# Performance work log

Hardware: AMD Instinct MI355X
Metric: run time of the kernel (lower is better)

Reference implementation:

```python
import jax, jax.numpy as jnp
import numpy as np

N = 20000   # nodes
E = 320000  # edges per relation
R = 4       # relations
H = 4       # attention heads
HID = 64    # hidden_dim1
DIN = 256   # input_dim
OUT = 64    # output_dim
NEG_SLOPE = 0.2  # PyG GATv2Conv default


def setup_inputs() -> dict:
    key = jax.random.key(0)
    ks = jax.random.split(key, 16)
    rn = lambda k, s: jax.random.normal(k, s, jnp.float32) * 0.05
    return {
        "x": jax.random.normal(ks[0], (N, DIN), jnp.float32),
        "edge_indices": jax.random.randint(ks[1], (R, 2, E), 0, N, jnp.int32),
        "Wl1": rn(ks[2], (R, DIN, H * HID)),
        "Wr1": rn(ks[3], (R, DIN, H * HID)),
        "att1": rn(ks[4], (R, H, HID)),
        "b1": rn(ks[5], (R, H * HID)),
        "Wl2": rn(ks[6], (R, H * HID, H * HID)),
        "Wr2": rn(ks[7], (R, H * HID, H * HID)),
        "att2": rn(ks[8], (R, H, HID)),
        "b2": rn(ks[9], (R, H * HID)),
        "Wrel3": rn(ks[10], (R, H * HID, HID)),
        "Wroot3": rn(ks[11], (R, H * HID, HID)),
        "b3": rn(ks[12], (R, HID)),
        "Wrel4": rn(ks[13], (R, HID, OUT)),
        "Wroot4": rn(ks[14], (R, HID, OUT)),
        "b4": rn(ks[15], (R, OUT)),
    }


def gatv2(x, src, dst, Wl, Wr, att, bias):
    """PyG GATv2Conv (concat heads, add_self_loops=True, share_weights=False)."""
    n = x.shape[0]
    loop = jnp.arange(n, dtype=src.dtype)
    src = jnp.concatenate([src, loop])  # add self loops
    dst = jnp.concatenate([dst, loop])
    xl = (x @ Wl).reshape(n, H, -1)  # source transform [N,H,C]
    xr = (x @ Wr).reshape(n, H, -1)  # target transform [N,H,C]
    z = jax.nn.leaky_relu(xl[src] + xr[dst], NEG_SLOPE)  # [E',H,C]
    e = jnp.einsum('ehc,hc->eh', z, att)                 # per-edge logits
    m = jax.ops.segment_max(e, dst, num_segments=n)
    m = jnp.where(jnp.isfinite(m), m, 0.0)
    p = jnp.exp(e - m[dst])
    s = jax.ops.segment_sum(p, dst, num_segments=n)
    alpha = p / s[dst]                                   # segment softmax
    out = jax.ops.segment_sum(alpha[:, :, None] * xl[src], dst, num_segments=n)
    return out.reshape(n, -1) + bias


def graphconv(x, src, dst, Wrel, Wroot, b):
    """PyG GraphConv: W1 x_i + W2 sum_j x_j (aggr='add')."""
    agg = jax.ops.segment_sum(x[src], dst, num_segments=x.shape[0])
    return agg @ Wrel + b + x @ Wroot


def reference(x, edge_indices, Wl1, Wr1, att1, b1, Wl2, Wr2, att2, b2,
              Wrel3, Wroot3, b3, Wrel4, Wroot4, b4):
    outs = []
    for i in range(R):  # small fixed relation count
        src, dst = edge_indices[i, 0], edge_indices[i, 1]
        h = jax.nn.relu(gatv2(x, src, dst, Wl1[i], Wr1[i], att1[i], b1[i]))
        h = jax.nn.relu(gatv2(h, src, dst, Wl2[i], Wr2[i], att2[i], b2[i]))
        h = jax.nn.relu(graphconv(h, src, dst, Wrel3[i], Wroot3[i], b3[i]))
        h = graphconv(h, src, dst, Wrel4[i], Wroot4[i], b4[i])
        outs.append(h[:, None, :])
    return jnp.concatenate(outs, axis=1)  # [N, R, OUT]
```

## Files before the change

kernel.cpp:

```cpp
#include <hip/hip_runtime.h>
#include <hip/hip_fp16.h>
#include <math.h>

#define NN   20000
#define EE   320000
#define RR   4
#define NBKT 4
#define BKTW 5000
#define SM   (NBKT*NN)
#define SB   40
#define SE   2000

typedef unsigned short u16;
typedef unsigned int   u32;
typedef _Float16 half8v __attribute__((ext_vector_type(8)));
typedef _Float16 v2h    __attribute__((ext_vector_type(2)));
typedef __attribute__((ext_vector_type(4))) float f32x4;

static __device__ __forceinline__ u16 f2h(float f){ return __half_as_ushort(__float2half_rn(f)); }
static __device__ __forceinline__ v2h u2v(u32 u){ union{u32 u; v2h v;} c; c.u=u; return c.v; }
static __device__ __forceinline__ u32 v2u(v2h v){ union{u32 u; v2h v;} c; c.v=v; return c.u; }
static __device__ __forceinline__ v2h splat2(float f){ v2h r; r[0]=(_Float16)f; r[1]=(_Float16)f; return r; }
static __device__ __forceinline__ float fdot2(v2h a, v2h b, float c){
  return __builtin_amdgcn_fdot2(a, b, c, false);
}
static __device__ __forceinline__ void gload_lds16(const void* g, void* l){
  __builtin_amdgcn_global_load_lds((const __attribute__((address_space(1))) void*)g,
                                   (__attribute__((address_space(3))) void*)l, 16, 0, 0);
}

__global__ void k_countA(const int* __restrict__ ei, int* __restrict__ degb){
  int i = blockIdx.x*blockDim.x + threadIdx.x;
  if (i < RR*EE) {
    int r = i / EE, e = i % EE;
    int s = ei[(size_t)r*2*EE + e];
    int d = ei[(size_t)r*2*EE + EE + e];
    int b = s / BKTW;
    atomicAdd(&degb[((size_t)r*NN + d)*NBKT + b], 1);
  }
}
__global__ __launch_bounds__(256) void k_scanA(const int* __restrict__ degb, int* __restrict__ bsum){
  int r = blockIdx.x / SB, b = blockIdx.x % SB;
  const int* p = degb + (size_t)r*SM + b*SE;
  int t = threadIdx.x;
  int s = 0;
  for (int i = t; i < SE; i += 256) s += p[i];
  s += __shfl_xor(s,1); s += __shfl_xor(s,2); s += __shfl_xor(s,4);
  s += __shfl_xor(s,8); s += __shfl_xor(s,16); s += __shfl_xor(s,32);
  __shared__ int ws[4];
  if ((t & 63) == 0) ws[t >> 6] = s;
  __syncthreads();
  if (t == 0) bsum[blockIdx.x] = ws[0] + ws[1] + ws[2] + ws[3];
}
__global__ void k_scanB(int* __restrict__ bsum, int* __restrict__ off_all){
  int r = blockIdx.x;
  if (threadIdx.x == 0) {
    int run = 0;
    for (int b = 0; b < SB; ++b) {
      int v = bsum[r*SB + b];
      bsum[r*SB + b] = run;
      run += v;
    }
    off_all[(size_t)r*(SM+1) + SM] = run;
  }
}
__global__ __launch_bounds__(256) void k_scanC(const int* __restrict__ degb, const int* __restrict__ bsum,
                                               int* __restrict__ off_all, int* __restrict__ cur_all){
  int r = blockIdx.x / SB, b = blockIdx.x % SB;
  const int* p = degb + (size_t)r*SM + b*SE;
  int* off = off_all + (size_t)r*(SM+1) + b*SE;
  int* cur = cur_all + (size_t)r*SM + b*SE;
  int t = threadIdx.x;
  int base_i = t*8;
  int v[8]; int tot = 0;
  if (base_i < SE) {
    #pragma unroll
    for (int j = 0; j < 8; ++j) { v[j] = p[base_i + j]; tot += v[j]; }
  }
  __shared__ int part[256];
  part[t] = tot;
  __syncthreads();
  for (int d = 1; d < 256; d <<= 1) {
    int u = (t >= d) ? part[t-d] : 0;
    __syncthreads();
    part[t] += u;
    __syncthreads();
  }
  if (base_i < SE) {
    int run = bsum[r*SB + b] + ((t == 0) ? 0 : part[t-1]);
    #pragma unroll
    for (int j = 0; j < 8; ++j) {
      off[base_i + j] = run;
      cur[base_i + j] = run;
      run += v[j];
    }
  }
}
__global__ void k_scatterM(const int* __restrict__ ei, int* __restrict__ curb, u32* __restrict__ csr4){
  int bid = blockIdx.x;
  int pass = bid / 5000;
  int i = (bid - pass*5000)*256 + threadIdx.x;
  int dlo = pass*5000, dhi = dlo + 5000;
  if (i < RR*EE) {
    int r = i / EE, e = i - r*EE;
    int d = ei[(size_t)r*2*EE + EE + e];
    if (d >= dlo && d < dhi) {
      int s = ei[(size_t)r*2*EE + e];
      int b = s / BKTW;
      int p = atomicAdd(&curb[((size_t)r*NN + d)*NBKT + b], 1);
      csr4[(size_t)r*EE + p] = (u32)s * 4096u;
    }
  }
}

__global__ void k_prepx(const float* __restrict__ x, u16* __restrict__ xbf, int* __restrict__ degb){
  int kind = blockIdx.y;
  int i = blockIdx.x*256 + threadIdx.x;
  if (kind == 0) {
    if (i < NN*256/4) {
      float4 v = reinterpret_cast<const float4*>(x)[i];
      ushort4 b;
      b.x = f2h(v.x); b.y = f2h(v.y); b.z = f2h(v.z); b.w = f2h(v.w);
      reinterpret_cast<ushort4*>(xbf)[i] = b;
    }
  } else {
    if (i < RR*SM) degb[i] = 0;
  }
}

__global__ __launch_bounds__(256) void k_wtrans(
    const float* __restrict__ A1, const float* __restrict__ B1, u16* __restrict__ D1,
    const float* __restrict__ A2, const float* __restrict__ B2, u16* __restrict__ D2,
    const float* __restrict__ A3, const float* __restrict__ B3, u16* __restrict__ D3,
    const float* __restrict__ A4, const float* __restrict__ B4, u16* __restrict__ D4)
{
  int kind = blockIdx.z;
  int K, N; const float *A, *B; u16* D;
  if (kind == 0)      { K=256; N=256; A=A1; B=B1; D=D1; }
  else if (kind == 1) { K=256; N=256; A=A2; B=B2; D=D2; }
  else if (kind == 2) { K=256; N=64;  A=A3; B=B3; D=D3; }
  else                { K=64;  N=64;  A=A4; B=B4; D=D4; }
  const int tiles_n = N >> 6;
  const int tiles = (K >> 6) * tiles_n;
  const int tile = blockIdx.x;
  if (tile >= tiles) return;
  const int r = blockIdx.y >> 1, half = blockIdx.y & 1;
  const float* S = half ? B : A;
  const int tk = tile / tiles_n, tn = tile % tiles_n;
  __shared__ u16 ts[64][66];
  const int t = threadIdx.x;
  #pragma unroll
  for (int i = 0; i < 16; ++i) {
    int lin = i*256 + t;
    int row = lin >> 6, col = lin & 63;
    ts[row][col] = f2h(S[((size_t)r*K + tk*64 + row)*N + tn*64 + col]);
  }
  __syncthreads();
  #pragma unroll
  for (int i = 0; i < 16; ++i) {
    int lin = i*256 + t;
    int nrow = lin >> 6, kcol = lin & 63;
    D[((size_t)r*2*N + half*N + tn*64 + nrow)*K + tk*64 + kcol] = ts[kcol][nrow];
  }
}

__global__ __launch_bounds__(256) void k_mfma(
    const u16* __restrict__ A, const u16* __restrict__ BT,
    int M, int K, u16* __restrict__ Cb, int ldc,
    long aZ, long btZ, long cZ, int nby, int nz)
{
  constexpr int BM = 128, BN = 128;
  constexpr int FI = 4, FJ = 4;
  constexpr int CH = 20;
  const int bid = blockIdx.x;
  const int xcd = bid & 7;
  const int u   = bid >> 3;
  const int nbz = nby*nz;
  const int byz = u % nbz;
  const int bxi = u / nbz;
  const int bx  = xcd*CH + bxi;
  const int bm  = bx * BM;
  if (bm >= M) return;
  const int by  = byz % nby;
  const int zz  = byz / nby;
  const int bn  = by * BN;
  A  += (size_t)zz*aZ;
  BT += (size_t)zz*btZ;
  Cb += (size_t)zz*cZ;

  __shared__ u16 As[BM*32];
  __shared__ u16 Bs[BN*32];
  const int t = threadIdx.x;
  const int lane = t & 63, wid = t >> 6;
  const int wr = wid >> 1, wc = wid & 1;
  const int lr = lane & 15, lk = lane >> 4;

  f32x4 acc[FI][FJ];
  #pragma unroll
  for (int i = 0; i < FI; ++i)
    #pragma unroll
    for (int j = 0; j < FJ; ++j) acc[i][j] = (f32x4)(0.f);

  const int nk = K >> 5;
  char* AsB = (char*)As;
  char* BsB = (char*)Bs;

  for (int s = 0; s < nk; ++s) {
    const int kk = s << 5;
    #pragma unroll
    for (int i = 0; i < 2; ++i) {
      int c = t + 256*i;
      int row = c >> 2, sub = c & 3;
      int lsub = sub ^ (row & 3);
      int grow = bm + row; if (grow >= M) grow = M - 1;
      gload_lds16(A + (size_t)grow*K + kk + lsub*8, AsB + c*16);
    }
    #pragma unroll
    for (int i = 0; i < 2; ++i) {
      int c = t + 256*i;
      int row = c >> 2, sub = c & 3;
      int lsub = sub ^ (row & 3);
      gload_lds16(BT + (size_t)(bn + row)*K + kk + lsub*8, BsB + c*16);
    }
    __syncthreads();
    half8v a[FI], b[FJ];
    #pragma unroll
    for (int i = 0; i < FI; ++i) {
      int row = wr*64 + i*16 + lr;
      int sub = lk ^ (row & 3);
      a[i] = *reinterpret_cast<half8v*>(AsB + row*64 + sub*16);
    }
    #pragma unroll
    for (int j = 0; j < FJ; ++j) {
      int col = wc*64 + j*16 + lr;
      int sub = lk ^ (col & 3);
      b[j] = *reinterpret_cast<half8v*>(BsB + col*64 + sub*16);
    }
    #pragma unroll
    for (int i = 0; i < FI; ++i)
      #pragma unroll
      for (int j = 0; j < FJ; ++j)
        acc[i][j] = __builtin_amdgcn_mfma_f32_16x16x32_f16(a[i], b[j], acc[i][j], 0, 0, 0);
    __syncthreads();
  }

  #pragma unroll
  for (int i = 0; i < FI; ++i) {
    #pragma unroll
    for (int j = 0; j < FJ; ++j) {
      int col = bn + wc*64 + j*16 + lr;
      #pragma unroll
      for (int q = 0; q < 4; ++q) {
        int row = bm + wr*64 + i*16 + lk*4 + q;
        if (row < M) Cb[(size_t)row*ldc + col] = f2h(acc[i][j][q]);
      }
    }
  }
}

__global__ __launch_bounds__(256) void k_gat(
    const u16* __restrict__ xlr,
    const float* __restrict__ att, const float* __restrict__ bias,
    const int* __restrict__ offb4, const u32* __restrict__ csr4,
    u16* __restrict__ out)
{
  const int bid = blockIdx.x;
  const int z = (bid & 7) >> 1;
  const int j4 = ((bid >> 3) << 1) | (bid & 1);
  const int node = j4*4 + (threadIdx.x >> 6);
  if (node >= NN) return;
  const int lane = threadIdx.x & 63;
  const int sl = lane & 31, sub = lane >> 5;
  const int* offb = offb4 + (size_t)z*(SM+1);
  const u32* csr = csr4 + (size_t)z*EE;
  u16* outp = out + (size_t)z*(size_t)NN*256;

  const int co = sl*8;
  const char* xc = (const char*)xlr + (size_t)z*1024 + co*2;
  const u16* selfrow = xlr + (size_t)z*512 + (size_t)node*2048;
  const v2h c02 = splat2(0.2f);
  const float L2E = 1.4426950408889634f;

  uint4 rx = *reinterpret_cast<const uint4*>(selfrow + 256 + co);
  v2h xr2[4] = {u2v(rx.x), u2v(rx.y), u2v(rx.z), u2v(rx.w)};
  v2h av2[4];
  {
    float4 q0 = *reinterpret_cast<const float4*>(att + z*256 + co);
    float4 q1 = *reinterpret_cast<const float4*>(att + z*256 + co + 4);
    av2[0][0]=(_Float16)(q0.x*L2E); av2[0][1]=(_Float16)(q0.y*L2E);
    av2[1][0]=(_Float16)(q0.z*L2E); av2[1][1]=(_Float16)(q0.w*L2E);
    av2[2][0]=(_Float16)(q1.x*L2E); av2[2][1]=(_Float16)(q1.y*L2E);
    av2[3][0]=(_Float16)(q1.z*L2E); av2[3][1]=(_Float16)(q1.w*L2E);
  }
  uint4 sx = *reinterpret_cast<const uint4*>(selfrow + co);
  v2h xs2[4] = {u2v(sx.x), u2v(sx.y), u2v(sx.z), u2v(sx.w)};
  float ps = 0.f;
  #pragma unroll
  for (int i = 0; i < 4; ++i) {
    v2h zz = xs2[i] + xr2[i];
    v2h lr = __builtin_elementwise_max(zz, zz*c02);
    ps = fdot2(av2[i], lr, ps);
  }
  ps += __shfl_xor(ps,1); ps += __shfl_xor(ps,2); ps += __shfl_xor(ps,4);
  float wsf = (sub == 0) ? exp2f(fminf(ps - 6.f, 12.f)) : 0.f;
  float s = wsf;
  v2h a2[4];
  {
    v2h w2 = splat2(wsf);
    #pragma unroll
    for (int i = 0; i < 4; ++i) a2[i] = w2*xs2[i];
  }

  const int e0 = offb[node*NBKT], e1 = offb[node*NBKT + NBKT];
  const int kfull = e0 + ((e1 - e0) & ~7);
  for (int k = e0; k < kfull; k += 8) {
    v2h xv[4][4];
    float p[4];
    #pragma unroll
    for (int j = 0; j < 4; ++j) {
      u32 boff = csr[k + 2*j + sub];
      uint4 v = *reinterpret_cast<const uint4*>(xc + boff);
      xv[j][0]=u2v(v.x); xv[j][1]=u2v(v.y); xv[j][2]=u2v(v.z); xv[j][3]=u2v(v.w);
      float pp = 0.f;
      #pragma unroll
      for (int i = 0; i < 4; ++i) {
        v2h zz = xv[j][i] + xr2[i];
        v2h lr = __builtin_elementwise_max(zz, zz*c02);
        pp = fdot2(av2[i], lr, pp);
      }
      p[j] = pp;
    }
    #pragma unroll
    for (int j = 0; j < 4; ++j) {
      p[j] += __shfl_xor(p[j],1);
      p[j] += __shfl_xor(p[j],2);
      p[j] += __shfl_xor(p[j],4);
    }
    float w[4];
    #pragma unroll
    for (int j = 0; j < 4; ++j) w[j] = exp2f(fminf(p[j] - 6.f, 12.f));
    s += (w[0] + w[1]) + (w[2] + w[3]);
    #pragma unroll
    for (int j = 0; j < 4; ++j) {
      v2h w2 = splat2(w[j]);
      #pragma unroll
      for (int i = 0; i < 4; ++i) a2[i] += w2*xv[j][i];
    }
  }
  for (int k = kfull; k < e1; k += 2) {
    int kk = k + sub;
    bool val = kk < e1;
    u32 boff = csr[val ? kk : e1-1];
    uint4 v = *reinterpret_cast<const uint4*>(xc + boff);
    v2h xv[4] = {u2v(v.x), u2v(v.y), u2v(v.z), u2v(v.w)};
    float pp = 0.f;
    #pragma unroll
    for (int i = 0; i < 4; ++i) {
      v2h zz = xv[i] + xr2[i];
      v2h lr = __builtin_elementwise_max(zz, zz*c02);
      pp = fdot2(av2[i], lr, pp);
    }
    pp += __shfl_xor(pp,1); pp += __shfl_xor(pp,2); pp += __shfl_xor(pp,4);
    float w = val ? exp2f(fminf(pp - 6.f, 12.f)) : 0.f;
    s += w;
    v2h w2 = splat2(w);
    #pragma unroll
    for (int i = 0; i < 4; ++i) a2[i] += w2*xv[i];
  }
  s += __shfl_xor(s, 32);
  #pragma unroll
  for (int i = 0; i < 4; ++i) {
    u32 t = (u32)__shfl_xor((int)v2u(a2[i]), 32);
    a2[i] += u2v(t);
  }
  float inv = 1.f / s;
  if (sub == 0) {
    float4 b0 = *reinterpret_cast<const float4*>(bias + z*256 + co);
    float4 b1 = *reinterpret_cast<const float4*>(bias + z*256 + co + 4);
    float bv[8] = {b0.x,b0.y,b0.z,b0.w,b1.x,b1.y,b1.z,b1.w};
    u32 o[4];
    #pragma unroll
    for (int i = 0; i < 4; ++i) {
      float lo = fmaxf((float)a2[i][0]*inv + bv[2*i],   0.f);
      float hi = fmaxf((float)a2[i][1]*inv + bv[2*i+1], 0.f);
      o[i] = (u32)f2h(lo) | ((u32)f2h(hi) << 16);
    }
    uint4 ov = {o[0], o[1], o[2], o[3]};
    *reinterpret_cast<uint4*>(outp + (size_t)node*256 + co) = ov;
  }
}

template<int RELU, int F32OUT>
__global__ __launch_bounds__(256) void k_aggp(
    const u16* __restrict__ C, const float* __restrict__ bias,
    const int* __restrict__ offb4, const u32* __restrict__ csr4,
    u16* __restrict__ outb, float* __restrict__ outf)
{
  const int bid = blockIdx.x;
  const int z = (bid & 7) >> 1;
  const int j4 = ((bid >> 3) << 1) | (bid & 1);
  const int node = j4*4 + (threadIdx.x >> 6);
  if (node >= NN) return;
  const int lane = threadIdx.x & 63;
  const int g = lane >> 4, sl = lane & 15;
  const u16* Cp = C + (size_t)z*(size_t)NN*128;
  const char* Cc = (const char*)Cp + sl*8;
  const int* offb = offb4 + (size_t)z*(SM+1);
  const u32* csr = csr4 + (size_t)z*EE;
  const int co = sl*4;
  v2h acc0 = splat2(0.f), acc1 = splat2(0.f);
  const int e0 = offb[node*NBKT], e1 = offb[node*NBKT + NBKT];
  const int kfull = e0 + ((e1 - e0) & ~7);
  for (int k = e0; k < kfull; k += 8) {
    #pragma unroll
    for (int j = 0; j < 2; ++j) {
      u32 boff = csr[k + 2*g + j] >> 4;
      uint2 v = *reinterpret_cast<const uint2*>(Cc + boff);
      acc0 += u2v(v.x);
      acc1 += u2v(v.y);
    }
  }
  for (int k = kfull; k < e1; k += 4) {
    int kk = k + g;
    bool val = kk < e1;
    u32 boff = csr[val ? kk : e1-1] >> 4;
    uint2 v = *reinterpret_cast<const uint2*>(Cc + boff);
    acc0 += u2v(val ? v.x : 0u);
    acc1 += u2v(val ? v.y : 0u);
  }
  float a0 = (float)acc0[0], a1 = (float)acc0[1];
  float a2 = (float)acc1[0], a3 = (float)acc1[1];
  a0 += __shfl_xor(a0,16); a1 += __shfl_xor(a1,16);
  a2 += __shfl_xor(a2,16); a3 += __shfl_xor(a3,16);
  a0 += __shfl_xor(a0,32); a1 += __shfl_xor(a1,32);
  a2 += __shfl_xor(a2,32); a3 += __shfl_xor(a3,32);
  if (g == 0) {
    uint2 q = *reinterpret_cast<const uint2*>(Cp + (size_t)node*128 + 64 + co);
    v2h q0 = u2v(q.x), q1 = u2v(q.y);
    float4 bv = *reinterpret_cast<const float4*>(bias + z*64 + co);
    float v0 = a0 + (float)q0[0] + bv.x;
    float v1 = a1 + (float)q0[1] + bv.y;
    float v2 = a2 + (float)q1[0] + bv.z;
    float v3 = a3 + (float)q1[1] + bv.w;
    if (RELU) {
      v0 = fmaxf(v0, 0.f); v1 = fmaxf(v1, 0.f);
      v2 = fmaxf(v2, 0.f); v3 = fmaxf(v3, 0.f);
    }
    if (F32OUT) {
      float4 o = {v0, v1, v2, v3};
      *reinterpret_cast<float4*>(outf + (size_t)node*256 + z*64 + co) = o;
    } else {
      uint2 o;
      o.x = (u32)f2h(v0) | ((u32)f2h(v1) << 16);
      o.y = (u32)f2h(v2) | ((u32)f2h(v3) << 16);
      *reinterpret_cast<uint2*>(outb + ((size_t)z*NN + node)*64 + co) = o;
    }
  }
}

extern "C" void kernel_launch(void* const* d_in, const int* in_sizes, int n_in,
                              void* d_out, int out_size, void* d_ws, size_t ws_size,
                              hipStream_t stream)
{
  const float* x      = (const float*)d_in[0];
  const int*   ei     = (const int*)  d_in[1];
  const float* Wl1    = (const float*)d_in[2];
  const float* Wr1    = (const float*)d_in[3];
  const float* att1   = (const float*)d_in[4];
  const float* b1     = (const float*)d_in[5];
  const float* Wl2    = (const float*)d_in[6];
  const float* Wr2    = (const float*)d_in[7];
  const float* att2   = (const float*)d_in[8];
  const float* b2     = (const float*)d_in[9];
  const float* Wrel3  = (const float*)d_in[10];
  const float* Wroot3 = (const float*)d_in[11];
  const float* b3     = (const float*)d_in[12];
  const float* Wrel4  = (const float*)d_in[13];
  const float* Wroot4 = (const float*)d_in[14];
  const float* b4     = (const float*)d_in[15];
  float* out = (float*)d_out;

  const dim3 thr(256);
  const size_t NB2048 = (size_t)NN*2048;
  const size_t NB256  = (size_t)NN*256;
  const size_t NB128  = (size_t)NN*128;
  const size_t NB64   = (size_t)NN*64;

  u16* XLR = (u16*)d_ws;
  u16* h   = XLR + NB2048;
  u16* xbf = h   + NB256*RR;
  u16* W1T = xbf + NB256;
  u16* W2T = W1T + (size_t)RR*512*256;
  u16* W3T = W2T + (size_t)RR*512*256;
  u16* W4T = W3T + (size_t)RR*128*256;
  int* degb = (int*)(W4T + (size_t)RR*128*64);
  int* offb = degb + (size_t)RR*SM;
  int* curb = offb + (size_t)RR*(SM+1);
  u32* csr4 = (u32*)(curb + (size_t)RR*SM);
  int* bsum = (int*)(csr4 + (size_t)RR*EE);
  u16* C34 = XLR;
  u16* h3b = XLR + NB128*RR;

  k_prepx <<<dim3(5000,2), thr, 0, stream>>>(x, xbf, degb);
  k_wtrans<<<dim3(16,8,4), thr, 0, stream>>>(Wl1, Wr1, W1T, Wl2, Wr2, W2T,
                                             Wrel3, Wroot3, W3T, Wrel4, Wroot4, W4T);

  k_countA <<<dim3((RR*EE+255)/256), thr, 0, stream>>>(ei, degb);
  k_scanA  <<<dim3(RR*SB), thr, 0, stream>>>(degb, bsum);
  k_scanB  <<<dim3(RR), dim3(64), 0, stream>>>(bsum, offb);
  k_scanC  <<<dim3(RR*SB), thr, 0, stream>>>(degb, bsum, offb, curb);
  k_scatterM<<<dim3(20000), thr, 0, stream>>>(ei, curb, csr4);

  const dim3 gNode(20000);
  k_mfma<<<dim3(8*20*16), thr, 0, stream>>>(xbf, W1T, NN, 256, XLR, 2048, 0, 0, 0, 16, 1);
  k_gat<<<gNode, thr, 0, stream>>>(XLR, att1, b1, offb, csr4, h);
  k_mfma<<<dim3(8*20*16), thr, 0, stream>>>(h, W2T, NN, 256, XLR, 2048,
                                            (long)NB256, 512*256, 512, 4, 4);
  k_gat<<<gNode, thr, 0, stream>>>(XLR, att2, b2, offb, csr4, h);
  k_mfma<<<dim3(8*20*4), thr, 0, stream>>>(h, W3T, NN, 256, C34, 128,
                                           (long)NB256, 128*256, (long)NB128, 1, 4);
  k_aggp<1,0><<<gNode, thr, 0, stream>>>(C34, b3, offb, csr4, h3b, nullptr);
  k_mfma<<<dim3(8*20*4), thr, 0, stream>>>(h3b, W4T, NN, 64, C34, 128,
                                           (long)NB64, 128*64, (long)NB128, 1, 4);
  k_aggp<0,1><<<gNode, thr, 0, stream>>>(C34, b4, offb, csr4, nullptr, out);
}
```

Measured before the change: 484.8 us.

## Merge prep kernels, fold scanB into scanC, use nontemporal loads/stores

Merges the x-to-fp16 conversion, degree-buffer clearing and weight transposition into one launch, and folds the serial block-offset scan into scanC, where thread 0 of each block sums the preceding block totals. Together these remove two kernel launches and a tiny single-threaded kernel from the dependency chain. It also switches some per-node loads and stores in the GAT and aggregation kernels to nontemporal builtins so streaming data bypasses cache retention. The risk is that each scanC block now rereads the block sums redundantly, and the nontemporal hints could hurt if that data is reused soon after.

```diff
diff --git a/kernel.cpp b/kernel.cpp
--- a/kernel.cpp
+++ b/kernel.cpp
@@ -15,6 +15,8 @@
 typedef unsigned int   u32;
 typedef _Float16 half8v __attribute__((ext_vector_type(8)));
 typedef _Float16 v2h    __attribute__((ext_vector_type(2)));
+typedef u32 u32x4 __attribute__((ext_vector_type(4)));
+typedef u32 u32x2 __attribute__((ext_vector_type(2)));
 typedef __attribute__((ext_vector_type(4))) float f32x4;
 
 static __device__ __forceinline__ u16 f2h(float f){ return __half_as_ushort(__float2half_rn(f)); }
@@ -27,6 +29,61 @@
 static __device__ __forceinline__ void gload_lds16(const void* g, void* l){
   __builtin_amdgcn_global_load_lds((const __attribute__((address_space(1))) void*)g,
                                    (__attribute__((address_space(3))) void*)l, 16, 0, 0);
+}
+
+__global__ __launch_bounds__(256) void k_prep(
+    const float* __restrict__ x, u16* __restrict__ xbf, int* __restrict__ degb,
+    const float* __restrict__ A1, const float* __restrict__ B1, u16* __restrict__ D1,
+    const float* __restrict__ A2, const float* __restrict__ B2, u16* __restrict__ D2,
+    const float* __restrict__ A3, const float* __restrict__ B3, u16* __restrict__ D3,
+    const float* __restrict__ A4, const float* __restrict__ B4, u16* __restrict__ D4)
+{
+  __shared__ u16 ts[64][66];
+  const int bid = blockIdx.x;
+  const int t = threadIdx.x;
+  if (bid < 10000) {
+    int kind = bid / 5000;
+    int i = (bid % 5000)*256 + t;
+    if (kind == 0) {
+      if (i < NN*256/4) {
+        float4 v = reinterpret_cast<const float4*>(x)[i];
+        ushort4 b;
+        b.x = f2h(v.x); b.y = f2h(v.y); b.z = f2h(v.z); b.w = f2h(v.w);
+        reinterpret_cast<ushort4*>(xbf)[i] = b;
+      }
+    } else {
+      if (i < RR*SM) degb[i] = 0;
+    }
+    return;
+  }
+  int wid = bid - 10000;
+  int kind, tile, y;
+  int K, N; const float *A, *B; u16* D;
+  if (wid < 128)      { kind=0; tile=wid & 15;        y=wid >> 4; }
+  else if (wid < 256) { kind=1; tile=(wid-128) & 15;  y=(wid-128) >> 4; }
+  else if (wid < 288) { kind=2; tile=(wid-256) & 3;   y=(wid-256) >> 2; }
+  else                { kind=3; tile=0;               y=wid-288; }
+  if (kind == 0)      { K=256; N=256; A=A1; B=B1; D=D1; }
+  else if (kind == 1) { K=256; N=256; A=A2; B=B2; D=D2; }
+  else if (kind == 2) { K=256; N=64;  A=A3; B=B3; D=D3; }
+  else                { K=64;  N=64;  A=A4; B=B4; D=D4; }
+  const int tiles_n = N >> 6;
+  const int r = y >> 1, half = y & 1;
+  const float* S = half ? B : A;
+  const int tk = tile / tiles_n, tn = tile % tiles_n;
+  #pragma unroll
+  for (int i = 0; i < 16; ++i) {
+    int lin = i*256 + t;
+    int row = lin >> 6, col = lin & 63;
+    ts[row][col] = f2h(S[((size_t)r*K + tk*64 + row)*N + tn*64 + col]);
+  }
+  __syncthreads();
+  #pragma unroll
+  for (int i = 0; i < 16; ++i) {
+    int lin = i*256 + t;
+    int nrow = lin >> 6, kcol = lin & 63;
+    D[((size_t)r*2*N + half*N + tn*64 + nrow)*K + tk*64 + kcol] = ts[kcol][nrow];
+  }
 }
 
 __global__ void k_countA(const int* __restrict__ ei, int* __restrict__ degb){
@@ -52,18 +109,6 @@
   __syncthreads();
   if (t == 0) bsum[blockIdx.x] = ws[0] + ws[1] + ws[2] + ws[3];
 }
-__global__ void k_scanB(int* __restrict__ bsum, int* __restrict__ off_all){
-  int r = blockIdx.x;
-  if (threadIdx.x == 0) {
-    int run = 0;
-    for (int b = 0; b < SB; ++b) {
-      int v = bsum[r*SB + b];
-      bsum[r*SB + b] = run;
-      run += v;
-    }
-    off_all[(size_t)r*(SM+1) + SM] = run;
-  }
-}
 __global__ __launch_bounds__(256) void k_scanC(const int* __restrict__ degb, const int* __restrict__ bsum,
                                                int* __restrict__ off_all, int* __restrict__ cur_all){
   int r = blockIdx.x / SB, b = blockIdx.x % SB;
@@ -71,14 +116,25 @@
   int* off = off_all + (size_t)r*(SM+1) + b*SE;
   int* cur = cur_all + (size_t)r*SM + b*SE;
   int t = threadIdx.x;
+  __shared__ int sbase;
+  if (t == 0) {
+    int base = 0, tot = 0;
+    for (int bb = 0; bb < SB; ++bb) {
+      int v = bsum[r*SB + bb];
+      if (bb < b) base += v;
+      tot += v;
+    }
+    sbase = base;
+    if (b == SB-1) off_all[(size_t)r*(SM+1) + SM] = tot;
+  }
   int base_i = t*8;
-  int v[8]; int tot = 0;
+  int v[8]; int tsum = 0;
   if (base_i < SE) {
     #pragma unroll
-    for (int j = 0; j < 8; ++j) { v[j] = p[base_i + j]; tot += v[j]; }
+    for (int j = 0; j < 8; ++j) { v[j] = p[base_i + j]; tsum += v[j]; }
   }
   __shared__ int part[256];
-  part[t] = tot;
+  part[t] = tsum;
   __syncthreads();
   for (int d = 1; d < 256; d <<= 1) {
     int u = (t >= d) ? part[t-d] : 0;
@@ -87,7 +143,7 @@
     __syncthreads();
   }
   if (base_i < SE) {
-    int run = bsum[r*SB + b] + ((t == 0) ? 0 : part[t-1]);
+    int run = sbase + ((t == 0) ? 0 : part[t-1]);
     #pragma unroll
     for (int j = 0; j < 8; ++j) {
       off[base_i + j] = run;
@@ -110,57 +166,6 @@
       int p = atomicAdd(&curb[((size_t)r*NN + d)*NBKT + b], 1);
       csr4[(size_t)r*EE + p] = (u32)s * 4096u;
     }
-  }
-}
-
-__global__ void k_prepx(const float* __restrict__ x, u16* __restrict__ xbf, int* __restrict__ degb){
-  int kind = blockIdx.y;
-  int i = blockIdx.x*256 + threadIdx.x;
-  if (kind == 0) {
-    if (i < NN*256/4) {
-      float4 v = reinterpret_cast<const float4*>(x)[i];
-      ushort4 b;
-      b.x = f2h(v.x); b.y = f2h(v.y); b.z = f2h(v.z); b.w = f2h(v.w);
-      reinterpret_cast<ushort4*>(xbf)[i] = b;
-    }
-  } else {
-    if (i < RR*SM) degb[i] = 0;
-  }
-}
-
-__global__ __launch_bounds__(256) void k_wtrans(
-    const float* __restrict__ A1, const float* __restrict__ B1, u16* __restrict__ D1,
-    const float* __restrict__ A2, const float* __restrict__ B2, u16* __restrict__ D2,
-    const float* __restrict__ A3, const float* __restrict__ B3, u16* __restrict__ D3,
-    const float* __restrict__ A4, const float* __restrict__ B4, u16* __restrict__ D4)
-{
-  int kind = blockIdx.z;
-  int K, N; const float *A, *B; u16* D;
-  if (kind == 0)      { K=256; N=256; A=A1; B=B1; D=D1; }
-  else if (kind == 1) { K=256; N=256; A=A2; B=B2; D=D2; }
-  else if (kind == 2) { K=256; N=64;  A=A3; B=B3; D=D3; }
-  else                { K=64;  N=64;  A=A4; B=B4; D=D4; }
-  const int tiles_n = N >> 6;
-  const int tiles = (K >> 6) * tiles_n;
-  const int tile = blockIdx.x;
-  if (tile >= tiles) return;
-  const int r = blockIdx.y >> 1, half = blockIdx.y & 1;
-  const float* S = half ? B : A;
-  const int tk = tile / tiles_n, tn = tile % tiles_n;
-  __shared__ u16 ts[64][66];
-  const int t = threadIdx.x;
-  #pragma unroll
-  for (int i = 0; i < 16; ++i) {
-    int lin = i*256 + t;
-    int row = lin >> 6, col = lin & 63;
-    ts[row][col] = f2h(S[((size_t)r*K + tk*64 + row)*N + tn*64 + col]);
-  }
-  __syncthreads();
-  #pragma unroll
-  for (int i = 0; i < 16; ++i) {
-    int lin = i*256 + t;
-    int nrow = lin >> 6, kcol = lin & 63;
-    D[((size_t)r*2*N + half*N + tn*64 + nrow)*K + tk*64 + kcol] = ts[kcol][nrow];
   }
 }
 
@@ -281,8 +286,8 @@
   const v2h c02 = splat2(0.2f);
   const float L2E = 1.4426950408889634f;
 
-  uint4 rx = *reinterpret_cast<const uint4*>(selfrow + 256 + co);
-  v2h xr2[4] = {u2v(rx.x), u2v(rx.y), u2v(rx.z), u2v(rx.w)};
+  u32x4 rx = __builtin_nontemporal_load(reinterpret_cast<const u32x4*>(selfrow + 256 + co));
+  v2h xr2[4] = {u2v(rx[0]), u2v(rx[1]), u2v(rx[2]), u2v(rx[3])};
   v2h av2[4];
   {
     float4 q0 = *reinterpret_cast<const float4*>(att + z*256 + co);
@@ -378,15 +383,14 @@
     float4 b0 = *reinterpret_cast<const float4*>(bias + z*256 + co);
     float4 b1 = *reinterpret_cast<const float4*>(bias + z*256 + co + 4);
     float bv[8] = {b0.x,b0.y,b0.z,b0.w,b1.x,b1.y,b1.z,b1.w};
-    u32 o[4];
+    u32x4 ov;
     #pragma unroll
     for (int i = 0; i < 4; ++i) {
       float lo = fmaxf((float)a2[i][0]*inv + bv[2*i],   0.f);
       float hi = fmaxf((float)a2[i][1]*inv + bv[2*i+1], 0.f);
-      o[i] = (u32)f2h(lo) | ((u32)f2h(hi) << 16);
-    }
-    uint4 ov = {o[0], o[1], o[2], o[3]};
-    *reinterpret_cast<uint4*>(outp + (size_t)node*256 + co) = ov;
+      ov[i] = (u32)f2h(lo) | ((u32)f2h(hi) << 16);
+    }
+    __builtin_nontemporal_store(ov, reinterpret_cast<u32x4*>(outp + (size_t)node*256 + co));
   }
 }
 
@@ -435,8 +439,8 @@
   a0 += __shfl_xor(a0,32); a1 += __shfl_xor(a1,32);
   a2 += __shfl_xor(a2,32); a3 += __shfl_xor(a3,32);
   if (g == 0) {
-    uint2 q = *reinterpret_cast<const uint2*>(Cp + (size_t)node*128 + 64 + co);
-    v2h q0 = u2v(q.x), q1 = u2v(q.y);
+    u32x2 q = __builtin_nontemporal_load(reinterpret_cast<const u32x2*>(Cp + (size_t)node*128 + 64 + co));
+    v2h q0 = u2v(q[0]), q1 = u2v(q[1]);
     float4 bv = *reinterpret_cast<const float4*>(bias + z*64 + co);
     float v0 = a0 + (float)q0[0] + bv.x;
     float v1 = a1 + (float)q0[1] + bv.y;
@@ -450,10 +454,10 @@
       float4 o = {v0, v1, v2, v3};
       *reinterpret_cast<float4*>(outf + (size_t)node*256 + z*64 + co) = o;
     } else {
-      uint2 o;
-      o.x = (u32)f2h(v0) | ((u32)f2h(v1) << 16);
-      o.y = (u32)f2h(v2) | ((u32)f2h(v3) << 16);
-      *reinterpret_cast<uint2*>(outb + ((size_t)z*NN + node)*64 + co) = o;
+      u32x2 o;
+      o[0] = (u32)f2h(v0) | ((u32)f2h(v1) << 16);
+      o[1] = (u32)f2h(v2) | ((u32)f2h(v3) << 16);
+      __builtin_nontemporal_store(o, reinterpret_cast<u32x2*>(outb + ((size_t)z*NN + node)*64 + co));
     }
   }
 }
@@ -501,13 +505,12 @@
   u16* C34 = XLR;
   u16* h3b = XLR + NB128*RR;
 
-  k_prepx <<<dim3(5000,2), thr, 0, stream>>>(x, xbf, degb);
-  k_wtrans<<<dim3(16,8,4), thr, 0, stream>>>(Wl1, Wr1, W1T, Wl2, Wr2, W2T,
-                                             Wrel3, Wroot3, W3T, Wrel4, Wroot4, W4T);
+  k_prep<<<dim3(10296), thr, 0, stream>>>(x, xbf, degb,
+                                          Wl1, Wr1, W1T, Wl2, Wr2, W2T,
+                                          Wrel3, Wroot3, W3T, Wrel4, Wroot4, W4T);
 
   k_countA <<<dim3((RR*EE+255)/256), thr, 0, stream>>>(ei, degb);
   k_scanA  <<<dim3(RR*SB), thr, 0, stream>>>(degb, bsum);
-  k_scanB  <<<dim3(RR), dim3(64), 0, stream>>>(bsum, offb);
   k_scanC  <<<dim3(RR*SB), thr, 0, stream>>>(degb, bsum, offb, curb);
   k_scatterM<<<dim3(20000), thr, 0, stream>>>(ei, curb, csr4);
 
```

After: 486.2 us. Within noise of the previous version (+0.3%).
